# Optimization experiments

Measured on AMD Instinct MI355X. Metric: run time of the kernel, lower is better.

The kernel has to match this reference:

```python
import jax, jax.numpy as jnp
import numpy as np

B, C, H, W = 4, 512, 28, 28
HEADS, K, DIL = 16, 7, 1
DH = C // HEADS
EPS = 1e-5


def _nbr_idx(n):
    # NATTEN-style clamped windows: near borders the window shifts to stay in-bounds.
    span = DIL * (K - 1) + 1
    start = np.clip(np.arange(n) - (K // 2) * DIL, 0, n - span)
    idx = start[:, None] + np.arange(K) * DIL              # [n, K] absolute neighbor indices
    rel = (idx - np.arange(n)[:, None]) // DIL + (K - 1)    # [n, K] rpb indices in [0, 2K-2]
    return jnp.asarray(idx), jnp.asarray(rel)


def _batchnorm(x, gamma, beta):
    # x: [B, C, H, W]; training-mode BN (batch statistics, biased variance)
    mean = x.mean(axis=(0, 2, 3), keepdims=True)
    var = x.var(axis=(0, 2, 3), keepdims=True)
    xn = (x - mean) * jax.lax.rsqrt(var + EPS)
    return xn * gamma[None, :, None, None] + beta[None, :, None, None]


def _neighborhood_attn(xh, qkv_w, qkv_b, proj_w, proj_b, rpb):
    # xh: [B, H, W, C]
    qkv = jnp.einsum('bijc,oc->bijo', xh, qkv_w) + qkv_b          # [B,H,W,3C]
    qkv = qkv.reshape(B, H, W, 3, HEADS, DH)
    q = qkv[..., 0, :, :].transpose(0, 3, 1, 2, 4)                 # [B,heads,H,W,dh]
    k = qkv[..., 1, :, :].transpose(0, 3, 1, 2, 4)
    v = qkv[..., 2, :, :].transpose(0, 3, 1, 2, 4)

    idx_r, rel_r = _nbr_idx(H)
    idx_c, rel_c = _nbr_idx(W)

    def gather(t):  # [B,heads,H,W,dh] -> [B,heads,H,W,K*K,dh]
        t = t[:, :, idx_r]                 # [B,heads,H,K,W,dh]
        t = t[:, :, :, :, idx_c]           # [B,heads,H,K,W,K,dh]
        t = t.transpose(0, 1, 2, 4, 3, 5, 6)
        return t.reshape(B, HEADS, H, W, K * K, DH)

    kg = gather(k)
    vg = gather(v)

    scale = DH ** -0.5
    logits = jnp.einsum('bhijd,bhijnd->bhijn', q * scale, kg)      # [B,heads,H,W,K*K]

    # relative position bias: rpb[h, rel_r[i,a], rel_c[j,b]]
    bias = rpb[:, rel_r]                   # [heads,H,K,2K-1]
    bias = bias[:, :, :, rel_c]            # [heads,H,K,W,K]
    bias = bias.transpose(0, 1, 3, 2, 4).reshape(HEADS, H, W, K * K)
    logits = logits + bias[None]

    attn = jax.nn.softmax(logits, axis=-1)
    out = jnp.einsum('bhijn,bhijnd->bhijd', attn, vg)              # [B,heads,H,W,dh]
    out = out.transpose(0, 2, 3, 1, 4).reshape(B, H, W, C)
    return jnp.einsum('bijc,oc->bijo', out, proj_w) + proj_b


def setup_inputs() -> dict:
    key = jax.random.key(0)
    ks = jax.random.split(key, 8)
    p = lambda k_, shp: (jax.random.normal(k_, shp, jnp.float32) * 0.02)
    return {
        'x': jax.random.normal(ks[0], (B, C, H, W), jnp.float32),
        'qkv_w': p(ks[1], (3 * C, C)), 'qkv_b': jnp.zeros((3 * C,), jnp.float32),
        'proj_w': p(ks[2], (C, C)), 'proj_b': jnp.zeros((C,), jnp.float32),
        'rpb': p(ks[3], (HEADS, 2 * K - 1, 2 * K - 1)),
        'w1': p(ks[4], (2 * C, C)), 'b1': jnp.zeros((2 * C,), jnp.float32),
        'w2': p(ks[5], (C, 2 * C)), 'b2': jnp.zeros((C,), jnp.float32),
        'g1': jnp.ones((C,), jnp.float32), 'be1': jnp.zeros((C,), jnp.float32),
        'g2': jnp.ones((C,), jnp.float32), 'be2': jnp.zeros((C,), jnp.float32),
    }


def reference(x, qkv_w, qkv_b, proj_w, proj_b, rpb, w1, b1, w2, b2, g1, be1, g2, be2):
    xh = x.transpose(0, 2, 3, 1)                                   # NCHW -> NHWC
    h = _neighborhood_attn(xh, qkv_w, qkv_b, proj_w, proj_b, rpb)
    h = h.transpose(0, 3, 1, 2)                                    # back to NCHW
    x1 = _batchnorm(x + h, g1, be1)
    # FFN: 1x1 conv (C -> 2C), exact GELU, 1x1 conv (2C -> C)
    t = jnp.einsum('bchw,oc->bohw', x1, w1) + b1[None, :, None, None]
    t = jax.nn.gelu(t, approximate=False)
    h2 = jnp.einsum('bchw,oc->bohw', t, w2) + b2[None, :, None, None]
    return _batchnorm(x1 + h2, g2, be2)
```

## Files before the change

### kernel.cpp

```cpp
#include <hip/hip_runtime.h>
#include <hip/hip_bf16.h>
#include <math.h>

#define BATCH 4
#define CCH   512
#define HWPIX 784
#define NPIX  3136
#define MPAD  3200
#define EPS   1e-5f

using f32x4  = __attribute__((ext_vector_type(4))) float;
using bf16x8 = __attribute__((ext_vector_type(8))) __bf16;

__device__ __forceinline__ short f2b(float f) {
    unsigned u = __float_as_uint(f);
    unsigned r = (u + 0x7FFFu + ((u >> 16) & 1u)) >> 16;
    return (short)r;
}
__device__ __forceinline__ unsigned pk2(float a, float b) {
    return (unsigned)(unsigned short)f2b(a) | ((unsigned)(unsigned short)f2b(b) << 16);
}
__device__ __forceinline__ float bl(unsigned u)  { return __uint_as_float(u << 16); }
__device__ __forceinline__ float bh(unsigned u)  { return __uint_as_float(u & 0xffff0000u); }
__device__ __forceinline__ float b16f(short s) {
    return __uint_as_float((unsigned)(unsigned short)s << 16);
}

__device__ __forceinline__ void gload_lds16(const void* g, void* l) {
    __builtin_amdgcn_global_load_lds((const __attribute__((address_space(1))) void*)g,
                                     (__attribute__((address_space(3))) void*)l, 16, 0, 0);
}

__global__ __launch_bounds__(256) void k_prep(const float* __restrict__ qkv_w,
                                              const float* __restrict__ proj_w,
                                              const float* __restrict__ w2,
                                              const float* __restrict__ x,
                                              short* __restrict__ Wb,
                                              short* __restrict__ xhb) {
    __shared__ float tile[32][33];
    const int bid = blockIdx.x;
    if (bid < 768) {
        int i = (bid * 256 + threadIdx.x) * 8;
        const float* src; int base;
        if (i < 786432)       { src = qkv_w;  base = 0; }
        else if (i < 1048576) { src = proj_w; base = 786432; }
        else                  { src = w2;     base = 1048576; }
        const float* p = src + (i - base);
        float4 va = *(const float4*)p;
        float4 vb = *(const float4*)(p + 4);
        uint4 o;
        o.x = pk2(va.x, va.y); o.y = pk2(va.z, va.w);
        o.z = pk2(vb.x, vb.y); o.w = pk2(vb.z, vb.w);
        *(uint4*)&Wb[i] = o;
        return;
    }
    const int t = bid - 768;
    const int b = t / 400, r = t % 400;
    const int c0 = (r / 25) * 32, p0 = (r % 25) * 32;
    const int tx = threadIdx.x & 31, ty = threadIdx.x >> 5;
    for (int i = ty; i < 32; i += 8) {
        int c = c0 + i, p = p0 + tx;
        tile[i][tx] = (p < HWPIX) ? x[((size_t)b * CCH + c) * HWPIX + p] : 0.f;
    }
    __syncthreads();
    for (int i = ty; i < 32; i += 8) {
        int p = p0 + i, c = c0 + tx;
        if (p < HWPIX) xhb[((size_t)b * HWPIX + p) * CCH + c] = f2b(tile[tx][i]);
    }
}

template<int BM, int BN, int N, int K, int EPI, int OUTB, int STATS, int NBY>
__global__ __launch_bounds__(512) void k_gemm_mfma(
        const short* __restrict__ A, const short* __restrict__ Bw,
        const float* __restrict__ bias, const short* __restrict__ resb,
        const float* __restrict__ ss,
        short* __restrict__ Cb, float* __restrict__ part) {
    constexpr int BK = 64;
    constexpr int KH = K / 2;
    constexpr int MR = BM / 32, NR = BN / 32;
    constexpr int AISS = BM / 32, BISS = BN / 32;
    constexpr int SCR = (BM / 2) * BN;
    __shared__ __align__(16) short As[2][BM * BK];
    __shared__ __align__(16) short Bs[2][BN * BK];
    const int nb3 = gridDim.x >> 3;
    const int eff = ((int)blockIdx.x & 7) * nb3 + ((int)blockIdx.x >> 3);
    const int bx = eff / NBY, by = eff % NBY;
    const int tid   = threadIdx.x;
    const int half  = tid >> 8;
    const int tid_h = tid & 255;
    const int wid2  = (tid >> 6) & 3;
    const int lane  = tid & 63;
    const int wr    = wid2 >> 1, wc = wid2 & 1;
    const int m0    = bx * BM, n0 = by * BN;
    const int srow  = tid_h >> 3;
    const int skcz  = (tid_h & 7) ^ (srow & 7);
    const int frow  = lane & 15;
    const int fk2   = (lane >> 4) * 16;

    f32x4 acc[MR][NR];
    const f32x4 vzero = {0.f, 0.f, 0.f, 0.f};
#pragma unroll
    for (int m = 0; m < MR; ++m)
#pragma unroll
        for (int n = 0; n < NR; ++n) acc[m][n] = vzero;

    const short* Ab = A  + (size_t)(m0 + srow) * K + skcz * 8 + half * KH;
    const short* Bb = Bw + (size_t)(n0 + srow) * K + skcz * 8 + half * KH;
    const char* Abase = (const char*)&As[half][0];
    const char* Bbase = (const char*)&Bs[half][0];

    for (int k0 = 0; k0 < KH; k0 += BK) {
#pragma unroll
        for (int it = 0; it < AISS; ++it)
            gload_lds16(Ab + (size_t)it * 32 * K + k0, &As[half][(it * 256 + wid2 * 64) * 8]);
#pragma unroll
        for (int it = 0; it < BISS; ++it)
            gload_lds16(Bb + (size_t)it * 32 * K + k0, &Bs[half][(it * 256 + wid2 * 64) * 8]);
        __syncthreads();
#pragma unroll
        for (int kk = 0; kk < 2; ++kk) {
            bf16x8 af[MR], bfr[NR];
#pragma unroll
            for (int m = 0; m < MR; ++m) {
                const int Ra = wr * (BM / 2) + m * 16 + frow;
                af[m] = *(const bf16x8*)(Abase + Ra * 128 + ((kk * 64 + fk2) ^ ((Ra & 7) << 4)));
            }
#pragma unroll
            for (int n = 0; n < NR; ++n) {
                const int Rb = wc * (BN / 2) + n * 16 + frow;
                bfr[n] = *(const bf16x8*)(Bbase + Rb * 128 + ((kk * 64 + fk2) ^ ((Rb & 7) << 4)));
            }
#pragma unroll
            for (int m = 0; m < MR; ++m)
#pragma unroll
                for (int n = 0; n < NR; ++n)
                    acc[m][n] = __builtin_amdgcn_mfma_f32_16x16x32_bf16(af[m], bfr[n], acc[m][n], 0, 0, 0);
        }
        __syncthreads();
    }

    const int crow0l = wr * (BM / 2) + (lane >> 4) * 4;
    const int ccol0l = wc * (BN / 2) + (lane & 15);
    float* scr = wr ? (float*)Bs : (float*)As;
    const int rbase = crow0l - wr * (BM / 2);
    if (half == 1) {
#pragma unroll
        for (int m = 0; m < MR; ++m)
#pragma unroll
            for (int n = 0; n < NR; ++n)
#pragma unroll
                for (int j = 0; j < 4; ++j)
                    scr[(rbase + m * 16 + j) * BN + ccol0l + n * 16] = acc[m][n][j];
    }
    __syncthreads();

    float ls[NR], ls2[NR];
#pragma unroll
    for (int n = 0; n < NR; ++n) { ls[n] = 0.f; ls2[n] = 0.f; }

    if (half == 0) {
#pragma unroll
        for (int m = 0; m < MR; ++m)
#pragma unroll
            for (int n = 0; n < NR; ++n)
#pragma unroll
                for (int j = 0; j < 4; ++j)
                    acc[m][n][j] += scr[(rbase + m * 16 + j) * BN + ccol0l + n * 16];
#pragma unroll
        for (int m = 0; m < MR; ++m) {
            const int row0 = m0 + crow0l + m * 16;
#pragma unroll
            for (int n = 0; n < NR; ++n) {
                const int col = n0 + ccol0l + n * 16;
                const float bv = bias[col];
#pragma unroll
                for (int j = 0; j < 4; ++j) {
                    const int row = row0 + j;
                    float v = acc[m][n][j] + bv;
                    if (EPI == 1) v = 0.5f * v * (1.0f + erff(v * 0.70710678118654752f));
                    if (EPI == 2) v += b16f(resb[(size_t)row * 512 + col]);
                    if (EPI == 3) v += fmaf(b16f(resb[(size_t)row * 512 + col]),
                                            ss[col], ss[CCH + col]);
                    if (OUTB) Cb[(size_t)row * N + col] = f2b(v);
                    if (STATS && row < NPIX) { ls[n] += v; ls2[n] = fmaf(v, v, ls2[n]); }
                }
            }
        }
    }
    if (STATS) {
        float* red  = (float*)Bs + SCR;
        float* red2 = red + 8 * BN;
        if (half == 0) {
            const int rrow = wr * 4 + (lane >> 4);
#pragma unroll
            for (int n = 0; n < NR; ++n) {
                int cslot = ccol0l + n * 16;
                red [rrow * BN + cslot] = ls[n];
                red2[rrow * BN + cslot] = ls2[n];
            }
        }
        __syncthreads();
        if (tid < BN) {
            float s = 0.f, s2 = 0.f;
#pragma unroll
            for (int r = 0; r < 8; ++r) { s += red[r * BN + tid]; s2 += red2[r * BN + tid]; }
            part[bx * N + n0 + tid]          = s;
            part[50 * N + bx * N + n0 + tid] = s2;
        }
    }
}

__global__ __launch_bounds__(256) void k_attn(const short* __restrict__ qkvb,
                                              const float* __restrict__ rpb,
                                              short* __restrict__ outb) {
    const int xcd = blockIdx.x & 7, bidx = blockIdx.x >> 3;
    const int eff = xcd * 98 + bidx;
    const int wid = threadIdx.x >> 6, lane = threadIdx.x & 63;
    const int pix = eff * 4 + wid;
    const int h = lane >> 2;
    const int choff = lane * 8;
    const unsigned upix = (unsigned)pix;
    const int j = upix % 28u;
    const unsigned t2 = upix / 28u;
    const int i = t2 % 28u;
    const int b = t2 / 28u;
    const int si = min(max(i - 3, 0), 21), sj = min(max(j - 3, 0), 21);
    const int oi = si - i + 6, oj = sj - j + 6;
    const int pbase = b * HWPIX + si * 28 + sj;

    float q[8];
    {
        uint4 qu = *(const uint4*)(qkvb + (size_t)pix * 1536 + choff);
        const float sc = 0.17677669529663687f;
        q[0] = bl(qu.x) * sc; q[1] = bh(qu.x) * sc;
        q[2] = bl(qu.y) * sc; q[3] = bh(qu.y) * sc;
        q[4] = bl(qu.z) * sc; q[5] = bh(qu.z) * sc;
        q[6] = bl(qu.w) * sc; q[7] = bh(qu.w) * sc;
    }
    const short* kbase = qkvb + (size_t)pbase * 1536 + 512 + choff;
    const float* rb = rpb + h * 169 + oi * 13 + oj;

    float l = 0.f;
    float o[8] = {0.f, 0.f, 0.f, 0.f, 0.f, 0.f, 0.f, 0.f};
#pragma unroll
    for (int kr = 0; kr < 7; ++kr) {
        const short* krow = kbase + kr * (28 * 1536);
        const float* brow = rb + kr * 13;
#pragma unroll
        for (int kc = 0; kc < 7; ++kc) {
            const short* p = krow + kc * 1536;
            uint4 ku = *(const uint4*)p;
            uint4 vu = *(const uint4*)(p + 512);
            float dot = q[0] * bl(ku.x);
            dot = fmaf(q[1], bh(ku.x), dot);
            dot = fmaf(q[2], bl(ku.y), dot);
            dot = fmaf(q[3], bh(ku.y), dot);
            dot = fmaf(q[4], bl(ku.z), dot);
            dot = fmaf(q[5], bh(ku.z), dot);
            dot = fmaf(q[6], bl(ku.w), dot);
            dot = fmaf(q[7], bh(ku.w), dot);
            dot += __shfl_xor(dot, 1);
            dot += __shfl_xor(dot, 2);
            float e = __expf(dot + brow[kc]);
            l += e;
            o[0] = fmaf(e, bl(vu.x), o[0]);
            o[1] = fmaf(e, bh(vu.x), o[1]);
            o[2] = fmaf(e, bl(vu.y), o[2]);
            o[3] = fmaf(e, bh(vu.y), o[3]);
            o[4] = fmaf(e, bl(vu.z), o[4]);
            o[5] = fmaf(e, bh(vu.z), o[5]);
            o[6] = fmaf(e, bl(vu.w), o[6]);
            o[7] = fmaf(e, bh(vu.w), o[7]);
        }
    }
    const float rs = 1.f / l;
    uint4 ov;
    ov.x = pk2(o[0] * rs, o[1] * rs);
    ov.y = pk2(o[2] * rs, o[3] * rs);
    ov.z = pk2(o[4] * rs, o[5] * rs);
    ov.w = pk2(o[6] * rs, o[7] * rs);
    *(uint4*)&outb[(size_t)pix * 512 + choff] = ov;
}

__global__ __launch_bounds__(256) void k_fold_w1(const float* __restrict__ part,
                                                 const float* __restrict__ g,
                                                 const float* __restrict__ be,
                                                 const float* __restrict__ w1,
                                                 const float* __restrict__ b1,
                                                 short* __restrict__ w1s,
                                                 float* __restrict__ b1c,
                                                 float* __restrict__ ssout) {
    __shared__ float ssc[CCH], ssh[CCH];
    const int tid = threadIdx.x;
    for (int cc = tid; cc < CCH; cc += 256) {
        float s = 0.f, s2 = 0.f;
        for (int p = 0; p < 50; ++p) {
            s  += part[p * CCH + cc];
            s2 += part[50 * CCH + p * CCH + cc];
        }
        float mean = s * (1.0f / NPIX);
        float var  = s2 * (1.0f / NPIX) - mean * mean;
        float rstd = rsqrtf(var + EPS);
        float sc = rstd * g[cc], sh = be[cc] - mean * sc;
        ssc[cc] = sc; ssh[cc] = sh;
        if (blockIdx.x == 0) { ssout[cc] = sc; ssout[CCH + cc] = sh; }
    }
    __syncthreads();
    const int wv = tid >> 6, lane = tid & 63;
    const int c = lane * 8;
    float4 sa = *(const float4*)&ssc[c], sb = *(const float4*)&ssc[c + 4];
    float4 ha = *(const float4*)&ssh[c], hb = *(const float4*)&ssh[c + 4];
    for (int r = 0; r < 4; ++r) {
        const int n = blockIdx.x * 16 + r * 4 + wv;
        const float* wrow = w1 + (size_t)n * CCH + c;
        float4 wa = *(const float4*)wrow, wb = *(const float4*)(wrow + 4);
        uint4 o;
        o.x = pk2(wa.x * sa.x, wa.y * sa.y);
        o.y = pk2(wa.z * sa.z, wa.w * sa.w);
        o.z = pk2(wb.x * sb.x, wb.y * sb.y);
        o.w = pk2(wb.z * sb.z, wb.w * sb.w);
        *(uint4*)&w1s[(size_t)n * CCH + c] = o;
        float p = wa.x * ha.x + wa.y * ha.y + wa.z * ha.z + wa.w * ha.w
                + wb.x * hb.x + wb.y * hb.y + wb.z * hb.z + wb.w * hb.w;
#pragma unroll
        for (int off = 32; off >= 1; off >>= 1) p += __shfl_xor(p, off);
        if (lane == 0) b1c[n] = b1[n] + p;
    }
}

__global__ __launch_bounds__(256) void k_bn2_out(const short* __restrict__ y,
                                                 const float* __restrict__ part,
                                                 const float* __restrict__ g,
                                                 const float* __restrict__ be,
                                                 float* __restrict__ out) {
    __shared__ float tile[32][33];
    __shared__ float red[2][8][32];
    __shared__ float ssc[32], ssh[32];
    const int b  = blockIdx.z;
    const int p0 = blockIdx.y * 32;
    const int c0 = blockIdx.x * 32;
    const int tx = threadIdx.x & 31, ty = threadIdx.x >> 5;
    {
        const int c = c0 + tx;
        float s = 0.f, s2 = 0.f;
        for (int p = ty; p < 50; p += 8) {
            s  += part[p * CCH + c];
            s2 += part[50 * CCH + p * CCH + c];
        }
        red[0][ty][tx] = s; red[1][ty][tx] = s2;
    }
    __syncthreads();
    if (ty == 0) {
        float s = 0.f, s2 = 0.f;
#pragma unroll
        for (int r = 0; r < 8; ++r) { s += red[0][r][tx]; s2 += red[1][r][tx]; }
        float mean = s * (1.0f / NPIX);
        float var  = s2 * (1.0f / NPIX) - mean * mean;
        float rstd = rsqrtf(var + EPS);
        float sc = rstd * g[c0 + tx];
        ssc[tx] = sc; ssh[tx] = be[c0 + tx] - mean * sc;
    }
    __syncthreads();
    for (int i = ty; i < 32; i += 8) {
        int p = p0 + i, c = c0 + tx;
        float v = 0.f;
        if (p < HWPIX) v = fmaf(b16f(y[((size_t)b * HWPIX + p) * CCH + c]), ssc[tx], ssh[tx]);
        tile[i][tx] = v;
    }
    __syncthreads();
    for (int i = ty; i < 32; i += 8) {
        int c = c0 + i, p = p0 + tx;
        if (p < HWPIX) out[((size_t)b * CCH + c) * HWPIX + p] = tile[tx][i];
    }
}

extern "C" void kernel_launch(void* const* d_in, const int* in_sizes, int n_in,
                              void* d_out, int out_size, void* d_ws, size_t ws_size,
                              hipStream_t stream) {
    const float* x      = (const float*)d_in[0];
    const float* qkv_w  = (const float*)d_in[1];
    const float* qkv_b  = (const float*)d_in[2];
    const float* proj_w = (const float*)d_in[3];
    const float* proj_b = (const float*)d_in[4];
    const float* rpb    = (const float*)d_in[5];
    const float* w1     = (const float*)d_in[6];
    const float* b1     = (const float*)d_in[7];
    const float* w2     = (const float*)d_in[8];
    const float* b2     = (const float*)d_in[9];
    const float* g1     = (const float*)d_in[10];
    const float* be1    = (const float*)d_in[11];
    const float* g2     = (const float*)d_in[12];
    const float* be2    = (const float*)d_in[13];
    float* out = (float*)d_out;

    float* ws    = (float*)d_ws;
    short* XHb   = (short*)(ws);
    short* QKVb  = (short*)(ws + 819200);
    short* Tb    = QKVb;
    short* ATTb  = (short*)(ws + 3276800);
    short* Y1b   = (short*)(ws + 4096000);
    short* Y2b   = (short*)(ws + 4915200);
    short* Wb    = (short*)(ws + 5734400);
    short* Wqkv  = Wb;
    short* Wproj = Wb + 786432;
    short* W2b   = Wb + 1048576;
    short* W1s   = Wb + 1572864;
    float* PART  = ws + 6782976;
    float* SS1   = ws + 6834176;
    float* B1c   = ws + 6835200;

    k_prep<<<2368, 256, 0, stream>>>(qkv_w, proj_w, w2, x, Wb, XHb);
    k_gemm_mfma<64, 128, 1536, 512, 0, 1, 0, 12>
        <<<600, 512, 0, stream>>>(XHb, Wqkv, qkv_b, nullptr, nullptr,
                                  QKVb, nullptr);
    k_attn<<<784, 256, 0, stream>>>(QKVb, rpb, ATTb);
    k_gemm_mfma<64, 64, 512, 512, 2, 1, 1, 8>
        <<<400, 512, 0, stream>>>(ATTb, Wproj, proj_b, XHb, nullptr,
                                  Y1b, PART);
    k_fold_w1<<<64, 256, 0, stream>>>(PART, g1, be1, w1, b1, W1s, B1c, SS1);
    k_gemm_mfma<64, 128, 1024, 512, 1, 1, 0, 8>
        <<<400, 512, 0, stream>>>(Y1b, W1s, B1c, nullptr, nullptr,
                                  Tb, nullptr);
    k_gemm_mfma<64, 64, 512, 1024, 3, 1, 1, 8>
        <<<400, 512, 0, stream>>>(Tb, W2b, b2, Y1b, SS1,
                                  Y2b, PART);
    k_bn2_out<<<dim3(16, 25, BATCH), 256, 0, stream>>>(Y2b, PART, g2, be2, out);
}
```

Before: 89.15 us.

## Drop intra-block split-K from MFMA GEMMs, use 256-thread blocks

The GEMM kernel previously split K across two 256-thread halves of a 512-thread block and reduced the partial accumulators through shared memory before the epilogue. It now uses one 256-thread block that walks the full K range with single LDS buffers, so the scratch reduction and its extra barrier go away and every thread runs the epilogue. In exchange each block issues twice as many serial K iterations with fewer waves per block to hide latency, and LDS use per block is halved, which may let more blocks share a CU.

```diff
diff --git a/kernel.cpp b/kernel.cpp
--- a/kernel.cpp
+++ b/kernel.cpp
@@ -70,32 +70,27 @@
 }
 
 template<int BM, int BN, int N, int K, int EPI, int OUTB, int STATS, int NBY>
-__global__ __launch_bounds__(512) void k_gemm_mfma(
+__global__ __launch_bounds__(256) void k_gemm_mfma(
         const short* __restrict__ A, const short* __restrict__ Bw,
         const float* __restrict__ bias, const short* __restrict__ resb,
         const float* __restrict__ ss,
         short* __restrict__ Cb, float* __restrict__ part) {
     constexpr int BK = 64;
-    constexpr int KH = K / 2;
     constexpr int MR = BM / 32, NR = BN / 32;
     constexpr int AISS = BM / 32, BISS = BN / 32;
-    constexpr int SCR = (BM / 2) * BN;
-    __shared__ __align__(16) short As[2][BM * BK];
-    __shared__ __align__(16) short Bs[2][BN * BK];
+    __shared__ __align__(16) short As[BM * BK];
+    __shared__ __align__(16) short Bs[BN * BK];
     const int nb3 = gridDim.x >> 3;
     const int eff = ((int)blockIdx.x & 7) * nb3 + ((int)blockIdx.x >> 3);
     const int bx = eff / NBY, by = eff % NBY;
-    const int tid   = threadIdx.x;
-    const int half  = tid >> 8;
-    const int tid_h = tid & 255;
-    const int wid2  = (tid >> 6) & 3;
-    const int lane  = tid & 63;
-    const int wr    = wid2 >> 1, wc = wid2 & 1;
-    const int m0    = bx * BM, n0 = by * BN;
-    const int srow  = tid_h >> 3;
-    const int skcz  = (tid_h & 7) ^ (srow & 7);
-    const int frow  = lane & 15;
-    const int fk2   = (lane >> 4) * 16;
+    const int tid  = threadIdx.x;
+    const int wid  = tid >> 6, lane = tid & 63;
+    const int wr   = wid >> 1, wc = wid & 1;
+    const int m0   = bx * BM, n0 = by * BN;
+    const int srow = tid >> 3;
+    const int skcz = (tid & 7) ^ (srow & 7);
+    const int frow = lane & 15;
+    const int fk2  = (lane >> 4) * 16;
 
     f32x4 acc[MR][NR];
     const f32x4 vzero = {0.f, 0.f, 0.f, 0.f};
@@ -104,18 +99,18 @@
 #pragma unroll
         for (int n = 0; n < NR; ++n) acc[m][n] = vzero;
 
-    const short* Ab = A  + (size_t)(m0 + srow) * K + skcz * 8 + half * KH;
-    const short* Bb = Bw + (size_t)(n0 + srow) * K + skcz * 8 + half * KH;
-    const char* Abase = (const char*)&As[half][0];
-    const char* Bbase = (const char*)&Bs[half][0];
-
-    for (int k0 = 0; k0 < KH; k0 += BK) {
+    const short* Ab = A  + (size_t)(m0 + srow) * K + skcz * 8;
+    const short* Bb = Bw + (size_t)(n0 + srow) * K + skcz * 8;
+    const char* Abase = (const char*)As;
+    const char* Bbase = (const char*)Bs;
+
+    for (int k0 = 0; k0 < K; k0 += BK) {
 #pragma unroll
         for (int it = 0; it < AISS; ++it)
-            gload_lds16(Ab + (size_t)it * 32 * K + k0, &As[half][(it * 256 + wid2 * 64) * 8]);
+            gload_lds16(Ab + (size_t)it * 32 * K + k0, &As[(it * 32 + srow) * BK + (tid & 7) * 8]);
 #pragma unroll
         for (int it = 0; it < BISS; ++it)
-            gload_lds16(Bb + (size_t)it * 32 * K + k0, &Bs[half][(it * 256 + wid2 * 64) * 8]);
+            gload_lds16(Bb + (size_t)it * 32 * K + k0, &Bs[(it * 32 + srow) * BK + (tid & 7) * 8]);
         __syncthreads();
 #pragma unroll
         for (int kk = 0; kk < 2; ++kk) {
@@ -139,65 +134,41 @@
         __syncthreads();
     }
 
-    const int crow0l = wr * (BM / 2) + (lane >> 4) * 4;
-    const int ccol0l = wc * (BN / 2) + (lane & 15);
-    float* scr = wr ? (float*)Bs : (float*)As;
-    const int rbase = crow0l - wr * (BM / 2);
-    if (half == 1) {
-#pragma unroll
-        for (int m = 0; m < MR; ++m)
-#pragma unroll
-            for (int n = 0; n < NR; ++n)
-#pragma unroll
-                for (int j = 0; j < 4; ++j)
-                    scr[(rbase + m * 16 + j) * BN + ccol0l + n * 16] = acc[m][n][j];
-    }
-    __syncthreads();
-
+    const int crow0 = m0 + wr * (BM / 2) + (lane >> 4) * 4;
+    const int ccol0 = n0 + wc * (BN / 2) + (lane & 15);
     float ls[NR], ls2[NR];
 #pragma unroll
     for (int n = 0; n < NR; ++n) { ls[n] = 0.f; ls2[n] = 0.f; }
 
-    if (half == 0) {
-#pragma unroll
-        for (int m = 0; m < MR; ++m)
-#pragma unroll
-            for (int n = 0; n < NR; ++n)
-#pragma unroll
-                for (int j = 0; j < 4; ++j)
-                    acc[m][n][j] += scr[(rbase + m * 16 + j) * BN + ccol0l + n * 16];
-#pragma unroll
-        for (int m = 0; m < MR; ++m) {
-            const int row0 = m0 + crow0l + m * 16;
-#pragma unroll
-            for (int n = 0; n < NR; ++n) {
-                const int col = n0 + ccol0l + n * 16;
-                const float bv = bias[col];
-#pragma unroll
-                for (int j = 0; j < 4; ++j) {
-                    const int row = row0 + j;
-                    float v = acc[m][n][j] + bv;
-                    if (EPI == 1) v = 0.5f * v * (1.0f + erff(v * 0.70710678118654752f));
-                    if (EPI == 2) v += b16f(resb[(size_t)row * 512 + col]);
-                    if (EPI == 3) v += fmaf(b16f(resb[(size_t)row * 512 + col]),
-                                            ss[col], ss[CCH + col]);
-                    if (OUTB) Cb[(size_t)row * N + col] = f2b(v);
-                    if (STATS && row < NPIX) { ls[n] += v; ls2[n] = fmaf(v, v, ls2[n]); }
-                }
+#pragma unroll
+    for (int m = 0; m < MR; ++m) {
+        const int row0 = crow0 + m * 16;
+#pragma unroll
+        for (int n = 0; n < NR; ++n) {
+            const int col = ccol0 + n * 16;
+            const float bv = bias[col];
+#pragma unroll
+            for (int j = 0; j < 4; ++j) {
+                const int row = row0 + j;
+                float v = acc[m][n][j] + bv;
+                if (EPI == 1) v = 0.5f * v * (1.0f + erff(v * 0.70710678118654752f));
+                if (EPI == 2) v += b16f(resb[(size_t)row * 512 + col]);
+                if (EPI == 3) v += fmaf(b16f(resb[(size_t)row * 512 + col]),
+                                        ss[col], ss[CCH + col]);
+                if (OUTB) Cb[(size_t)row * N + col] = f2b(v);
+                if (STATS && row < NPIX) { ls[n] += v; ls2[n] = fmaf(v, v, ls2[n]); }
             }
         }
     }
     if (STATS) {
-        float* red  = (float*)Bs + SCR;
+        float* red  = (float*)Bs;
         float* red2 = red + 8 * BN;
-        if (half == 0) {
-            const int rrow = wr * 4 + (lane >> 4);
-#pragma unroll
-            for (int n = 0; n < NR; ++n) {
-                int cslot = ccol0l + n * 16;
-                red [rrow * BN + cslot] = ls[n];
-                red2[rrow * BN + cslot] = ls2[n];
-            }
+        const int rrow = wr * 4 + (lane >> 4);
+#pragma unroll
+        for (int n = 0; n < NR; ++n) {
+            const int cslot = wc * (BN / 2) + n * 16 + (lane & 15);
+            red [rrow * BN + cslot] = ls[n];
+            red2[rrow * BN + cslot] = ls2[n];
         }
         __syncthreads();
         if (tid < BN) {
@@ -411,18 +382,18 @@
 
     k_prep<<<2368, 256, 0, stream>>>(qkv_w, proj_w, w2, x, Wb, XHb);
     k_gemm_mfma<64, 128, 1536, 512, 0, 1, 0, 12>
-        <<<600, 512, 0, stream>>>(XHb, Wqkv, qkv_b, nullptr, nullptr,
+        <<<600, 256, 0, stream>>>(XHb, Wqkv, qkv_b, nullptr, nullptr,
                                   QKVb, nullptr);
     k_attn<<<784, 256, 0, stream>>>(QKVb, rpb, ATTb);
     k_gemm_mfma<64, 64, 512, 512, 2, 1, 1, 8>
-        <<<400, 512, 0, stream>>>(ATTb, Wproj, proj_b, XHb, nullptr,
+        <<<400, 256, 0, stream>>>(ATTb, Wproj, proj_b, XHb, nullptr,
                                   Y1b, PART);
     k_fold_w1<<<64, 256, 0, stream>>>(PART, g1, be1, w1, b1, W1s, B1c, SS1);
     k_gemm_mfma<64, 128, 1024, 512, 1, 1, 0, 8>
-        <<<400, 512, 0, stream>>>(Y1b, W1s, B1c, nullptr, nullptr,
+        <<<400, 256, 0, stream>>>(Y1b, W1s, B1c, nullptr, nullptr,
                                   Tb, nullptr);
     k_gemm_mfma<64, 64, 512, 1024, 3, 1, 1, 8>
-        <<<400, 512, 0, stream>>>(Tb, W2b, b2, Y1b, SS1,
+        <<<400, 256, 0, stream>>>(Tb, W2b, b2, Y1b, SS1,
                                   Y2b, PART);
     k_bn2_out<<<dim3(16, 25, BATCH), 256, 0, stream>>>(Y2b, PART, g2, be2, out);
 }
```

Measured after the change: 93.86 us (median of 3 runs). 1.05x slower.
